# Performance work log

Measured on AMD Instinct MI355X. Metric: run time of the kernel, lower is better.

## Reference

```python
import jax, jax.numpy as jnp
import numpy as np

B, T, C, H = 8, 2048, 512, 512


def setup_inputs() -> dict:
    key = jax.random.key(0)
    ks = jax.random.split(key, 9)
    s = 1.0 / np.sqrt(C)
    return {
        "q": jax.random.normal(ks[0], (B, T, C), jnp.float32),
        "k": jax.random.normal(ks[1], (B, T, C), jnp.float32),
        "v": jax.random.normal(ks[2], (B, T, C), jnp.float32),
        "Wq": jax.random.normal(ks[3], (C, H), jnp.float32) * s,
        "bq": jax.random.normal(ks[4], (H,), jnp.float32) * 0.01,
        "Wk": jax.random.normal(ks[5], (C, H), jnp.float32) * s,
        "bk": jax.random.normal(ks[6], (H,), jnp.float32) * 0.01,
        "Wv": jax.random.normal(ks[7], (C, H), jnp.float32) * s,
        "bv": jax.random.normal(ks[8], (H,), jnp.float32) * 0.01,
    }


def reference(q, k, v, Wq, bq, Wk, bk, Wv, bv):
    # Linear projections (Real_Linear == nn.Linear): [B,T,C] @ [C,H] + [H]
    query = jnp.einsum('btc,ch->bth', q, Wq) + bq
    key_p = jnp.einsum('btc,ch->bth', k, Wk) + bk
    value = jnp.einsum('btc,ch->bth', v, Wv) + bv
    # energy = Q @ K^T / sqrt(H)  -> [B, T, T]
    energy = jnp.einsum('bth,byh->bty', query, key_p) / jnp.sqrt(jnp.asarray(H, query.dtype))
    attn = jax.nn.softmax(energy, axis=-1)
    # weighted value: [B, T, T] @ [B, T, H] -> [B, T, H]
    return jnp.einsum('bty,byh->bth', attn, value)
```

## Files before the change

### kernel.cpp

```cpp
#include <hip/hip_runtime.h>
#include <hip/hip_bf16.h>

typedef unsigned short u16;
typedef unsigned int u32;
typedef short s16x8 __attribute__((ext_vector_type(8)));
typedef float f32x4 __attribute__((ext_vector_type(4)));

#define NB 8
#define NT 2048
#define NC 512
#define NH 512

__device__ __forceinline__ u16 f2bf(float f) {
  unsigned u = __float_as_uint(f);
  u += 0x7FFFu + ((u >> 16) & 1u);
  return (u16)(u >> 16);
}

__device__ __forceinline__ void gld16(const u16* src, u16* lds_dst) {
  __builtin_amdgcn_global_load_lds(
      (const __attribute__((address_space(1))) u32*)src,
      (__attribute__((address_space(3))) u32*)lds_dst, 16, 0, 0);
}

__global__ __launch_bounds__(256) void wt_kernel(const float* __restrict__ Wq,
                                                 const float* __restrict__ Wk,
                                                 const float* __restrict__ Wv,
                                                 u16* __restrict__ WqT,
                                                 u16* __restrict__ WkT,
                                                 u16* __restrict__ WvT) {
  __shared__ float tile[32][33];
  const float* W = (blockIdx.z == 0) ? Wq : (blockIdx.z == 1) ? Wk : Wv;
  u16* WT = (blockIdx.z == 0) ? WqT : (blockIdx.z == 1) ? WkT : WvT;
  const int x = threadIdx.x & 31;
  const int y = threadIdx.x >> 5;
  const int k0 = blockIdx.x * 32, h0 = blockIdx.y * 32;
#pragma unroll
  for (int p = 0; p < 4; ++p)
    tile[y + 8 * p][x] = W[(size_t)(k0 + y + 8 * p) * NH + h0 + x];
  __syncthreads();
#pragma unroll
  for (int p = 0; p < 4; ++p)
    WT[(size_t)(h0 + y + 8 * p) * NC + k0 + x] = f2bf(tile[x][y + 8 * p]);
}

__global__ __launch_bounds__(256) void proj_kernel(const float* __restrict__ Xq,
                                                   const float* __restrict__ Xk,
                                                   const float* __restrict__ Xv,
                                                   const u16* __restrict__ WqT,
                                                   const u16* __restrict__ WkT,
                                                   const u16* __restrict__ WvT,
                                                   const float* __restrict__ bq,
                                                   const float* __restrict__ bk,
                                                   const float* __restrict__ bv,
                                                   u16* __restrict__ Yq,
                                                   u16* __restrict__ Yk,
                                                   u16* __restrict__ Yv) {
  __shared__ __align__(16) u16 Asub[2][128 * 40];
  __shared__ __align__(16) u16 Bsub[2][128 * 40];
  const int zz = blockIdx.z;
  const float* X = (zz == 0) ? Xq : (zz == 1) ? Xk : Xv;
  const u16* WT = (zz == 0) ? WqT : (zz == 1) ? WkT : WvT;
  const float* bias = (zz == 0) ? bq : (zz == 1) ? bk : bv;
  u16* Y = (zz == 0) ? Yq : (zz == 1) ? Yk : Yv;

  const int t = threadIdx.x;
  const int lane = t & 63;
  const int w = t >> 6;
  const int l16 = lane & 15;
  const int ko8 = (lane >> 4) * 8;
  const int m0 = blockIdx.y * 128;
  const int n0 = blockIdx.x * 128;
  const int wr = (w >> 1) * 64, wc = (w & 1) * 64;
  f32x4 acc[4][4] = {};

  float4 areg[4];
  int4 breg[2];
#define PLOAD(kt)                                                              \
  {                                                                            \
    const int k0_ = (kt) * 32;                                                 \
    _Pragma("unroll")                                                          \
    for (int p = 0; p < 4; ++p) {                                              \
      int c = t + 256 * p;                                                     \
      areg[p] = *(const float4*)&X[(size_t)(m0 + (c >> 3)) * NC + k0_ + (c & 7) * 4]; \
    }                                                                          \
    _Pragma("unroll")                                                          \
    for (int p = 0; p < 2; ++p) {                                              \
      int c = t + 256 * p;                                                     \
      breg[p] = *(const int4*)&WT[(size_t)(n0 + (c >> 2)) * NC + k0_ + (c & 3) * 8];  \
    }                                                                          \
  }
#define PWRITE(buf)                                                            \
  {                                                                            \
    _Pragma("unroll")                                                          \
    for (int p = 0; p < 4; ++p) {                                              \
      int c = t + 256 * p;                                                     \
      ushort4 bb;                                                              \
      bb.x = f2bf(areg[p].x); bb.y = f2bf(areg[p].y);                          \
      bb.z = f2bf(areg[p].z); bb.w = f2bf(areg[p].w);                          \
      *(ushort4*)&Asub[buf][(c >> 3) * 40 + (c & 7) * 4] = bb;                 \
    }                                                                          \
    _Pragma("unroll")                                                          \
    for (int p = 0; p < 2; ++p) {                                              \
      int c = t + 256 * p;                                                     \
      *(int4*)&Bsub[buf][(c >> 2) * 40 + (c & 3) * 8] = breg[p];               \
    }                                                                          \
  }

  PLOAD(0)
  PWRITE(0)
  __syncthreads();

  int pb = 0;
  for (int kt = 0; kt < 16; ++kt) {
    if (kt < 15) PLOAD(kt + 1)
    s16x8 af[4], bf[4];
#pragma unroll
    for (int i = 0; i < 4; ++i)
      af[i] = *(const s16x8*)&Asub[pb][(wr + i * 16 + l16) * 40 + ko8];
#pragma unroll
    for (int j = 0; j < 4; ++j)
      bf[j] = *(const s16x8*)&Bsub[pb][(wc + j * 16 + l16) * 40 + ko8];
#pragma unroll
    for (int i = 0; i < 4; ++i)
#pragma unroll
      for (int j = 0; j < 4; ++j)
        acc[i][j] = __builtin_amdgcn_mfma_f32_16x16x32_bf16(af[i], bf[j], acc[i][j], 0, 0, 0);
    if (kt < 15) PWRITE(pb ^ 1)
    __syncthreads();
    pb ^= 1;
  }
#undef PLOAD
#undef PWRITE
  const int rg = (lane >> 4) * 4;
#pragma unroll
  for (int i = 0; i < 4; ++i)
#pragma unroll
    for (int j = 0; j < 4; ++j) {
      const int col = n0 + wc + j * 16 + l16;
      const float bcol = bias[col];
#pragma unroll
      for (int jj = 0; jj < 4; ++jj) {
        const int row = m0 + wr + i * 16 + rg + jj;
        Y[(size_t)row * NH + col] = f2bf(acc[i][j][jj] + bcol);
      }
    }
}

__global__ __launch_bounds__(256) void vt_kernel(const u16* __restrict__ Vp,
                                                 u16* __restrict__ VpT) {
  __shared__ u16 tile[32][33];
  const int x = threadIdx.x & 31;
  const int y = threadIdx.x >> 5;
  const int t0 = blockIdx.x * 32, h0 = blockIdx.y * 32, b = blockIdx.z;
  const u16* src = Vp + (size_t)b * NT * NH;
  u16* dst = VpT + (size_t)b * NH * NT;
#pragma unroll
  for (int p = 0; p < 4; ++p)
    tile[y + 8 * p][x] = src[(size_t)(t0 + y + 8 * p) * NH + h0 + x];
  __syncthreads();
#pragma unroll
  for (int p = 0; p < 4; ++p)
    dst[(size_t)(h0 + y + 8 * p) * NT + t0 + x] = tile[x][y + 8 * p];
}

__global__ __launch_bounds__(512, 2) void flash_partial(const u16* __restrict__ Qp,
                                                        const u16* __restrict__ Kp,
                                                        const u16* __restrict__ VpT,
                                                        float* __restrict__ O0,
                                                        float* __restrict__ O1,
                                                        float* __restrict__ mlws) {
  __shared__ __align__(16) u16 Klds[2][32 * 512];
  __shared__ __align__(16) u16 Vlds[2][32 * 512];

  const int t = threadIdx.x;
  const int lane = t & 63;
  const int w = t >> 6;
  const int l16 = lane & 15;
  const int g = lane >> 4;
  const int g8 = g * 8;
  const int b = blockIdx.x;
  const int q0 = blockIdx.y * 128;
  const int z = blockIdx.z;
  const int qg = q0 + w * 16 + l16;
  const int kperm = (l16 >> 2) * 8 + (l16 & 3);
  const float kscale = 0.044194173824159216f;

  s16x8 qf[16];
  {
    const u16* qrow = Qp + (size_t)(b * NT + qg) * NH;
#pragma unroll
    for (int ks = 0; ks < 16; ++ks)
      qf[ks] = *(const s16x8*)&qrow[ks * 32 + g8];
  }

  f32x4 oacc[32] = {};
  float m_run = -1e30f, l_run = 0.f;

  const u16* kbat = Kp + (size_t)(b * NT + z * 1024) * NH;
  const u16* vbat = VpT + (size_t)b * NH * NT + z * 1024;

#define STAGE(buf, it)                                                         \
  {                                                                            \
    _Pragma("unroll")                                                          \
    for (int r = 0; r < 4; ++r) {                                              \
      const int i = w * 4 + r;                                      \
      gld16(kbat + (size_t)((it) * 32 + kperm + ((i & 1) << 2)) * NH           \
                 + ((i >> 1) << 5) + g8,                                       \
            &Klds[buf][i * 512]);                                              \
      gld16(vbat + (size_t)(i * 16 + l16) * NT + (it) * 32 + g8,               \
            &Vlds[buf][i * 512]);                                              \
    }                                                                          \
  }

  STAGE(0, 0)
  __syncthreads();

  int pb = 0;
  for (int it = 0; it < 32; ++it) {
    if (it < 31) STAGE(pb ^ 1, it + 1)
    f32x4 s0a = {}, s0b = {}, s1a = {}, s1b = {};
    __builtin_amdgcn_s_setprio(1);
#pragma unroll
    for (int ks = 0; ks < 8; ++ks) {
      s16x8 kf0 = *(const s16x8*)&Klds[pb][(ks * 2 + 0) * 512 + lane * 8];
      s16x8 kf1 = *(const s16x8*)&Klds[pb][(ks * 2 + 1) * 512 + lane * 8];
      s16x8 kf2 = *(const s16x8*)&Klds[pb][((ks + 8) * 2 + 0) * 512 + lane * 8];
      s16x8 kf3 = *(const s16x8*)&Klds[pb][((ks + 8) * 2 + 1) * 512 + lane * 8];
      s0a = __builtin_amdgcn_mfma_f32_16x16x32_bf16(kf0, qf[ks], s0a, 0, 0, 0);
      s1a = __builtin_amdgcn_mfma_f32_16x16x32_bf16(kf1, qf[ks], s1a, 0, 0, 0);
      s0b = __builtin_amdgcn_mfma_f32_16x16x32_bf16(kf2, qf[ks + 8], s0b, 0, 0, 0);
      s1b = __builtin_amdgcn_mfma_f32_16x16x32_bf16(kf3, qf[ks + 8], s1b, 0, 0, 0);
    }
    __builtin_amdgcn_s_setprio(0);
    const f32x4 s0 = s0a + s0b;
    const f32x4 s1 = s1a + s1b;
    float pv[8];
#pragma unroll
    for (int j = 0; j < 4; ++j) { pv[j] = s0[j] * kscale; pv[4 + j] = s1[j] * kscale; }
    float mx = pv[0];
#pragma unroll
    for (int j = 1; j < 8; ++j) mx = fmaxf(mx, pv[j]);
    mx = fmaxf(mx, __shfl_xor(mx, 16, 64));
    mx = fmaxf(mx, __shfl_xor(mx, 32, 64));
    if (__any(mx > m_run + 8.f)) {
      const float m_new = fmaxf(m_run, mx);
      const float scale = __expf(m_run - m_new);
#pragma unroll
      for (int ht = 0; ht < 32; ++ht) {
        oacc[ht][0] *= scale; oacc[ht][1] *= scale;
        oacc[ht][2] *= scale; oacc[ht][3] *= scale;
      }
      l_run *= scale;
      m_run = m_new;
    }
    float ts = 0.f;
#pragma unroll
    for (int j = 0; j < 8; ++j) { pv[j] = __expf(pv[j] - m_run); ts += pv[j]; }
    l_run += ts;
    union { u32 u[4]; s16x8 v; } pf;
    pf.u[0] = ((u32)f2bf(pv[1]) << 16) | f2bf(pv[0]);
    pf.u[1] = ((u32)f2bf(pv[3]) << 16) | f2bf(pv[2]);
    pf.u[2] = ((u32)f2bf(pv[5]) << 16) | f2bf(pv[4]);
    pf.u[3] = ((u32)f2bf(pv[7]) << 16) | f2bf(pv[6]);
    __builtin_amdgcn_s_setprio(1);
#pragma unroll
    for (int ht = 0; ht < 32; ++ht) {
      s16x8 vf = *(const s16x8*)&Vlds[pb][ht * 512 + lane * 8];
      oacc[ht] = __builtin_amdgcn_mfma_f32_16x16x32_bf16(vf, pf.v, oacc[ht], 0, 0, 0);
    }
    __builtin_amdgcn_s_setprio(0);
    __syncthreads();
    pb ^= 1;
  }
  float* obase = (z ? O1 : O0) + (size_t)(b * NT + qg) * NH;
#pragma unroll
  for (int ht = 0; ht < 32; ++ht) {
    float4 st;
    st.x = oacc[ht][0]; st.y = oacc[ht][1];
    st.z = oacc[ht][2]; st.w = oacc[ht][3];
    *(float4*)&obase[ht * 16 + g * 4] = st;
  }
  float lt = l_run;
  lt += __shfl_xor(lt, 16, 64);
  lt += __shfl_xor(lt, 32, 64);
  if (g == 0) {
    const size_t row = (size_t)b * NT + qg;
    mlws[row * 4 + z * 2 + 0] = m_run;
    mlws[row * 4 + z * 2 + 1] = lt;
  }
#undef STAGE
}

__global__ __launch_bounds__(128) void merge_kernel(float* __restrict__ out,
                                                    const float* __restrict__ O1,
                                                    const float* __restrict__ mlws) {
  const size_t row = blockIdx.x;
  const float m0 = mlws[row * 4 + 0], l0 = mlws[row * 4 + 1];
  const float m1 = mlws[row * 4 + 2], l1 = mlws[row * 4 + 3];
  const float m = fmaxf(m0, m1);
  const float a0 = __expf(m0 - m), a1 = __expf(m1 - m);
  const float inv = 1.f / (a0 * l0 + a1 * l1);
  const float c0 = a0 * inv, c1 = a1 * inv;
  const size_t idx = row * NH + threadIdx.x * 4;
  float4 o0 = *(const float4*)&out[idx];
  float4 o1 = *(const float4*)&O1[idx];
  float4 r;
  r.x = c0 * o0.x + c1 * o1.x;
  r.y = c0 * o0.y + c1 * o1.y;
  r.z = c0 * o0.z + c1 * o1.z;
  r.w = c0 * o0.w + c1 * o1.w;
  *(float4*)&out[idx] = r;
}

__global__ __launch_bounds__(256, 1) void flash_kernel(const u16* __restrict__ Qp,
                                                       const u16* __restrict__ Kp,
                                                       const u16* __restrict__ VpT,
                                                       float* __restrict__ out) {
  __shared__ __align__(16) u16 Klds[2][32 * 512];
  __shared__ __align__(16) u16 Vlds[2][32 * 512];

  const int t = threadIdx.x;
  const int lane = t & 63;
  const int w = t >> 6;
  const int l16 = lane & 15;
  const int g = lane >> 4;
  const int g8 = g * 8;
  const int b = blockIdx.x;
  const int q0 = blockIdx.y * 64;
  const int qg = q0 + w * 16 + l16;
  const int kperm = (l16 >> 2) * 8 + (l16 & 3);
  const float kscale = 0.044194173824159216f;

  s16x8 qf[16];
  {
    const u16* qrow = Qp + (size_t)(b * NT + qg) * NH;
#pragma unroll
    for (int ks = 0; ks < 16; ++ks)
      qf[ks] = *(const s16x8*)&qrow[ks * 32 + g8];
  }
  f32x4 oacc[32] = {};
  float m_run = -1e30f, l_run = 0.f;
  const u16* kbat = Kp + (size_t)b * NT * NH;
  const u16* vbat = VpT + (size_t)b * NH * NT;

#pragma unroll
  for (int r = 0; r < 8; ++r) {
    const int i = w * 8 + r;
    gld16(kbat + (size_t)(kperm + ((i & 1) << 2)) * NH + ((i >> 1) << 5) + g8,
          &Klds[0][i * 512]);
    gld16(vbat + (size_t)(i * 16 + l16) * NT + g8, &Vlds[0][i * 512]);
  }
  __syncthreads();

  int pb = 0;
  for (int it = 0; it < 64; ++it) {
    if (it < 63) {
      const int kv1 = (it + 1) * 32;
      const int nb = pb ^ 1;
#pragma unroll
      for (int r = 0; r < 8; ++r) {
        const int i = w * 8 + r;
        gld16(kbat + (size_t)(kv1 + kperm + ((i & 1) << 2)) * NH + ((i >> 1) << 5) + g8,
              &Klds[nb][i * 512]);
        gld16(vbat + (size_t)(i * 16 + l16) * NT + kv1 + g8, &Vlds[nb][i * 512]);
      }
    }
    f32x4 s0 = {}, s1 = {};
#pragma unroll
    for (int ks = 0; ks < 16; ++ks) {
      s16x8 kf0 = *(const s16x8*)&Klds[pb][(ks * 2 + 0) * 512 + lane * 8];
      s16x8 kf1 = *(const s16x8*)&Klds[pb][(ks * 2 + 1) * 512 + lane * 8];
      s0 = __builtin_amdgcn_mfma_f32_16x16x32_bf16(kf0, qf[ks], s0, 0, 0, 0);
      s1 = __builtin_amdgcn_mfma_f32_16x16x32_bf16(kf1, qf[ks], s1, 0, 0, 0);
    }
    float pv[8];
#pragma unroll
    for (int j = 0; j < 4; ++j) { pv[j] = s0[j] * kscale; pv[4 + j] = s1[j] * kscale; }
    float mx = pv[0];
#pragma unroll
    for (int j = 1; j < 8; ++j) mx = fmaxf(mx, pv[j]);
    mx = fmaxf(mx, __shfl_xor(mx, 16, 64));
    mx = fmaxf(mx, __shfl_xor(mx, 32, 64));
    if (__any(mx > m_run + 8.f)) {
      const float m_new = fmaxf(m_run, mx);
      const float scale = __expf(m_run - m_new);
#pragma unroll
      for (int ht = 0; ht < 32; ++ht) {
        oacc[ht][0] *= scale; oacc[ht][1] *= scale;
        oacc[ht][2] *= scale; oacc[ht][3] *= scale;
      }
      l_run *= scale;
      m_run = m_new;
    }
    float ts = 0.f;
#pragma unroll
    for (int j = 0; j < 8; ++j) { pv[j] = __expf(pv[j] - m_run); ts += pv[j]; }
    l_run += ts;
    union { u32 u[4]; s16x8 v; } pf;
    pf.u[0] = ((u32)f2bf(pv[1]) << 16) | f2bf(pv[0]);
    pf.u[1] = ((u32)f2bf(pv[3]) << 16) | f2bf(pv[2]);
    pf.u[2] = ((u32)f2bf(pv[5]) << 16) | f2bf(pv[4]);
    pf.u[3] = ((u32)f2bf(pv[7]) << 16) | f2bf(pv[6]);
#pragma unroll
    for (int ht = 0; ht < 32; ++ht) {
      s16x8 vf = *(const s16x8*)&Vlds[pb][ht * 512 + lane * 8];
      oacc[ht] = __builtin_amdgcn_mfma_f32_16x16x32_bf16(vf, pf.v, oacc[ht], 0, 0, 0);
    }
    __syncthreads();
    pb ^= 1;
  }
  float lt = l_run;
  lt += __shfl_xor(lt, 16, 64);
  lt += __shfl_xor(lt, 32, 64);
  const float inv = 1.f / lt;
  float* obase = out + (size_t)(b * NT + qg) * NH;
#pragma unroll
  for (int ht = 0; ht < 32; ++ht) {
    float4 st;
    st.x = oacc[ht][0] * inv; st.y = oacc[ht][1] * inv;
    st.z = oacc[ht][2] * inv; st.w = oacc[ht][3] * inv;
    *(float4*)&obase[ht * 16 + g * 4] = st;
  }
}

extern "C" void kernel_launch(void* const* d_in, const int* in_sizes, int n_in,
                              void* d_out, int out_size, void* d_ws, size_t ws_size,
                              hipStream_t stream) {
  (void)in_sizes; (void)n_in; (void)out_size;
  const float* q  = (const float*)d_in[0];
  const float* k  = (const float*)d_in[1];
  const float* v  = (const float*)d_in[2];
  const float* Wq = (const float*)d_in[3];
  const float* bq = (const float*)d_in[4];
  const float* Wk = (const float*)d_in[5];
  const float* bk = (const float*)d_in[6];
  const float* Wv = (const float*)d_in[7];
  const float* bv = (const float*)d_in[8];
  float* out = (float*)d_out;

  u16* ws   = (u16*)d_ws;
  u16* WqT  = ws;
  u16* WkT  = WqT + (size_t)NC * NH;
  u16* WvT  = WkT + (size_t)NC * NH;
  u16* Qp   = WvT + (size_t)NC * NH;
  u16* Kp   = Qp + (size_t)NB * NT * NH;
  u16* Vp   = Kp + (size_t)NB * NT * NH;
  u16* VpT  = Vp + (size_t)NB * NT * NH;
  u16* endb = VpT + (size_t)NB * NT * NH;
  float* O1   = (float*)endb;
  float* mlws = O1 + (size_t)NB * NT * NH;
  const size_t need = (size_t)((char*)(mlws + (size_t)NB * NT * 4) - (char*)d_ws);

  wt_kernel<<<dim3(16, 16, 3), 256, 0, stream>>>(Wq, Wk, Wv, WqT, WkT, WvT);

  proj_kernel<<<dim3(4, 128, 3), 256, 0, stream>>>(q, k, v, WqT, WkT, WvT,
                                                   bq, bk, bv, Qp, Kp, Vp);

  vt_kernel<<<dim3(64, 16, NB), 256, 0, stream>>>(Vp, VpT);

  if (ws_size >= need) {
    flash_partial<<<dim3(NB, NT / 128, 2), 512, 0, stream>>>(Qp, Kp, VpT, out, O1, mlws);
    merge_kernel<<<dim3(NB * NT), 128, 0, stream>>>(out, O1, mlws);
  } else {
    flash_kernel<<<dim3(NB, NT / 64), 256, 0, stream>>>(Qp, Kp, VpT, out);
  }
}
```

Baseline: 217.3 us.

## Retile projection GEMM to full-width rows with async weight staging to LDS

The projection kernel moves from 128x128 output tiles to 64-row tiles that cover all 512 output columns. Each fp32 input row is therefore read and converted to bf16 once rather than four times, and weight tiles are staged into LDS with global_load_lds in an MFMA-fragment-ordered layout. In the flash kernel, the cross-lane max shuffles are moved inside the rescale branch, so they are skipped when no lane exceeds the running-max threshold. The tradeoff is a larger per-thread accumulator (128 floats) and a larger LDS footprint, which may limit occupancy; the launch bound now asks for 2 blocks per CU.

Measured after the change: 254.2 us. 17.0% more time.

```diff
diff --git a/kernel.cpp b/kernel.cpp
--- a/kernel.cpp
+++ b/kernel.cpp
@@ -44,20 +44,20 @@
     WT[(size_t)(h0 + y + 8 * p) * NC + k0 + x] = f2bf(tile[x][y + 8 * p]);
 }
 
-__global__ __launch_bounds__(256) void proj_kernel(const float* __restrict__ Xq,
-                                                   const float* __restrict__ Xk,
-                                                   const float* __restrict__ Xv,
-                                                   const u16* __restrict__ WqT,
-                                                   const u16* __restrict__ WkT,
-                                                   const u16* __restrict__ WvT,
-                                                   const float* __restrict__ bq,
-                                                   const float* __restrict__ bk,
-                                                   const float* __restrict__ bv,
-                                                   u16* __restrict__ Yq,
-                                                   u16* __restrict__ Yk,
-                                                   u16* __restrict__ Yv) {
-  __shared__ __align__(16) u16 Asub[2][128 * 40];
-  __shared__ __align__(16) u16 Bsub[2][128 * 40];
+__global__ __launch_bounds__(256, 2) void proj_kernel(const float* __restrict__ Xq,
+                                                      const float* __restrict__ Xk,
+                                                      const float* __restrict__ Xv,
+                                                      const u16* __restrict__ WqT,
+                                                      const u16* __restrict__ WkT,
+                                                      const u16* __restrict__ WvT,
+                                                      const float* __restrict__ bq,
+                                                      const float* __restrict__ bk,
+                                                      const float* __restrict__ bv,
+                                                      u16* __restrict__ Yq,
+                                                      u16* __restrict__ Yk,
+                                                      u16* __restrict__ Yv) {
+  __shared__ __align__(16) u16 Asub[2][64 * 40];
+  __shared__ __align__(16) u16 Bsub[2][32 * 512];
   const int zz = blockIdx.z;
   const float* X = (zz == 0) ? Xq : (zz == 1) ? Xk : Xv;
   const u16* WT = (zz == 0) ? WqT : (zz == 1) ? WkT : WvT;
@@ -68,80 +68,83 @@
   const int lane = t & 63;
   const int w = t >> 6;
   const int l16 = lane & 15;
-  const int ko8 = (lane >> 4) * 8;
-  const int m0 = blockIdx.y * 128;
-  const int n0 = blockIdx.x * 128;
-  const int wr = (w >> 1) * 64, wc = (w & 1) * 64;
-  f32x4 acc[4][4] = {};
-
-  float4 areg[4];
-  int4 breg[2];
-#define PLOAD(kt)                                                              \
+  const int g = lane >> 4;
+  const int g8 = g * 8;
+  const int ko8 = g8;
+  const int m0 = blockIdx.x * 64;
+  f32x4 acc[4][8] = {};
+
+  float4 areg[2];
+#define PLOAD_A(kt)                                                            \
   {                                                                            \
     const int k0_ = (kt) * 32;                                                 \
     _Pragma("unroll")                                                          \
-    for (int p = 0; p < 4; ++p) {                                              \
+    for (int p = 0; p < 2; ++p) {                                              \
       int c = t + 256 * p;                                                     \
       areg[p] = *(const float4*)&X[(size_t)(m0 + (c >> 3)) * NC + k0_ + (c & 7) * 4]; \
     }                                                                          \
+  }
+#define PWRITE_A(buf)                                                          \
+  {                                                                            \
     _Pragma("unroll")                                                          \
     for (int p = 0; p < 2; ++p) {                                              \
-      int c = t + 256 * p;                                                     \
-      breg[p] = *(const int4*)&WT[(size_t)(n0 + (c >> 2)) * NC + k0_ + (c & 3) * 8];  \
-    }                                                                          \
-  }
-#define PWRITE(buf)                                                            \
-  {                                                                            \
-    _Pragma("unroll")                                                          \
-    for (int p = 0; p < 4; ++p) {                                              \
       int c = t + 256 * p;                                                     \
       ushort4 bb;                                                              \
       bb.x = f2bf(areg[p].x); bb.y = f2bf(areg[p].y);                          \
       bb.z = f2bf(areg[p].z); bb.w = f2bf(areg[p].w);                          \
       *(ushort4*)&Asub[buf][(c >> 3) * 40 + (c & 7) * 4] = bb;                 \
     }                                                                          \
+  }
+#define STAGE_B(buf, kt)                                                       \
+  {                                                                            \
     _Pragma("unroll")                                                          \
-    for (int p = 0; p < 2; ++p) {                                              \
-      int c = t + 256 * p;                                                     \
-      *(int4*)&Bsub[buf][(c >> 2) * 40 + (c & 3) * 8] = breg[p];               \
+    for (int r = 0; r < 8; ++r) {                                              \
+      const int f = w * 8 + r;                                                 \
+      gld16(WT + (size_t)(f * 16 + l16) * NC + (kt) * 32 + g8,                 \
+            &Bsub[buf][f * 512]);                                              \
     }                                                                          \
   }
 
-  PLOAD(0)
-  PWRITE(0)
+  PLOAD_A(0)
+  PWRITE_A(0)
+  STAGE_B(0, 0)
   __syncthreads();
 
   int pb = 0;
   for (int kt = 0; kt < 16; ++kt) {
-    if (kt < 15) PLOAD(kt + 1)
-    s16x8 af[4], bf[4];
+    if (kt < 15) {
+      PLOAD_A(kt + 1)
+      STAGE_B(pb ^ 1, kt + 1)
+    }
+    s16x8 af[4], bf[8];
 #pragma unroll
     for (int i = 0; i < 4; ++i)
-      af[i] = *(const s16x8*)&Asub[pb][(wr + i * 16 + l16) * 40 + ko8];
-#pragma unroll
-    for (int j = 0; j < 4; ++j)
-      bf[j] = *(const s16x8*)&Bsub[pb][(wc + j * 16 + l16) * 40 + ko8];
+      af[i] = *(const s16x8*)&Asub[pb][(i * 16 + l16) * 40 + ko8];
+#pragma unroll
+    for (int j = 0; j < 8; ++j)
+      bf[j] = *(const s16x8*)&Bsub[pb][(w * 8 + j) * 512 + lane * 8];
 #pragma unroll
     for (int i = 0; i < 4; ++i)
 #pragma unroll
-      for (int j = 0; j < 4; ++j)
+      for (int j = 0; j < 8; ++j)
         acc[i][j] = __builtin_amdgcn_mfma_f32_16x16x32_bf16(af[i], bf[j], acc[i][j], 0, 0, 0);
-    if (kt < 15) PWRITE(pb ^ 1)
+    if (kt < 15) PWRITE_A(pb ^ 1)
     __syncthreads();
     pb ^= 1;
   }
-#undef PLOAD
-#undef PWRITE
-  const int rg = (lane >> 4) * 4;
+#undef PLOAD_A
+#undef PWRITE_A
+#undef STAGE_B
+  const int rg = g * 4;
 #pragma unroll
   for (int i = 0; i < 4; ++i)
 #pragma unroll
-    for (int j = 0; j < 4; ++j) {
-      const int col = n0 + wc + j * 16 + l16;
+    for (int j = 0; j < 8; ++j) {
+      const int col = w * 128 + j * 16 + l16;
       const float bcol = bias[col];
 #pragma unroll
       for (int jj = 0; jj < 4; ++jj) {
-        const int row = m0 + wr + i * 16 + rg + jj;
+        const int row = m0 + i * 16 + rg + jj;
         Y[(size_t)row * NH + col] = f2bf(acc[i][j][jj] + bcol);
       }
     }
@@ -238,12 +241,12 @@
     float pv[8];
 #pragma unroll
     for (int j = 0; j < 4; ++j) { pv[j] = s0[j] * kscale; pv[4 + j] = s1[j] * kscale; }
-    float mx = pv[0];
-#pragma unroll
-    for (int j = 1; j < 8; ++j) mx = fmaxf(mx, pv[j]);
-    mx = fmaxf(mx, __shfl_xor(mx, 16, 64));
-    mx = fmaxf(mx, __shfl_xor(mx, 32, 64));
-    if (__any(mx > m_run + 8.f)) {
+    float mxl = pv[0];
+#pragma unroll
+    for (int j = 1; j < 8; ++j) mxl = fmaxf(mxl, pv[j]);
+    if (__any(mxl > m_run + 8.f)) {
+      float mx = fmaxf(mxl, __shfl_xor(mxl, 16, 64));
+      mx = fmaxf(mx, __shfl_xor(mx, 32, 64));
       const float m_new = fmaxf(m_run, mx);
       const float scale = __expf(m_run - m_new);
 #pragma unroll
@@ -454,8 +457,8 @@
 
   wt_kernel<<<dim3(16, 16, 3), 256, 0, stream>>>(Wq, Wk, Wv, WqT, WkT, WvT);
 
-  proj_kernel<<<dim3(4, 128, 3), 256, 0, stream>>>(q, k, v, WqT, WkT, WvT,
-                                                   bq, bk, bv, Qp, Kp, Vp);
+  proj_kernel<<<dim3(NB * NT / 64, 1, 3), 256, 0, stream>>>(q, k, v, WqT, WkT, WvT,
+                                                            bq, bk, bv, Qp, Kp, Vp);
 
   vt_kernel<<<dim3(64, 16, NB), 256, 0, stream>>>(Vp, VpT);
 
```
